# Kernel tuning notes

Measured on AMD Instinct MI355X. Metric: run time of the kernel, lower is better.

## Reference

```python
import jax, jax.numpy as jnp
import numpy as np

EPS = float(np.finfo(np.float32).eps)

# (joint_id, joint_name, parent_name) in the module's fkm_computation_order
ORDER = [
    (1, 'rHip', 'hip'), (2, 'rKnee', 'rHip'), (3, 'rAnkle', 'rKnee'), (4, 'rToe', 'rAnkle'),
    (6, 'lHip', 'hip'), (7, 'lKnee', 'lHip'), (8, 'lAnkle', 'lKnee'), (9, 'lToe', 'lAnkle'),
    (11, 'spine', 'hip'), (12, 'spine1', 'spine'), (13, 'thorax', 'spine1'), (14, 'neck', 'thorax'),
    (15, 'head', 'neck'), (16, 'lShoulderAnchor', 'spine1'), (17, 'lShoulder', 'lShoulderAnchor'),
    (18, 'lElbow', 'lShoulder'), (19, 'lWrist', 'lElbow'), (20, 'lThumb', 'lWrist'),
    (22, 'lWristEnd', 'lWrist'), (24, 'rShoulderAnchor', 'spine1'), (25, 'rShoulder', 'rShoulderAnchor'),
    (26, 'rElbow', 'rShoulder'), (27, 'rWrist', 'rElbow'), (28, 'rThumb', 'rWrist'),
    (30, 'rWristEnd', 'rWrist'),
]


def axis_angle_to_matrix(a):
    """Rodrigues formula, batched. a: [B,3] -> [B,3,3]."""
    theta = jnp.linalg.norm(a, axis=-1, keepdims=True)  # [B,1]
    r = a / (theta + EPS)                               # [B,3]
    r0, r1, r2 = r[:, 0], r[:, 1], r[:, 2]
    z = jnp.zeros_like(r0)
    # skew-symmetric S with S[0,1]=-r2, S[0,2]=r1, S[1,2]=-r0 (as in torch code)
    S = jnp.stack([
        jnp.stack([z, -r2, r1], axis=-1),
        jnp.stack([r2, z, -r0], axis=-1),
        jnp.stack([-r1, r0, z], axis=-1),
    ], axis=-2)  # [B,3,3]
    th = theta[..., None]  # [B,1,1]
    I = jnp.eye(3, dtype=a.dtype)
    return I + jnp.sin(th) * S + (1.0 - jnp.cos(th)) * (S @ S)


def setup_inputs() -> dict:
    key = jax.random.key(0)
    k1, k2 = jax.random.split(key)
    B = 262144
    x = jax.random.normal(k1, (B, 99), dtype=jnp.float32)
    offset = jax.random.normal(k2, (32, 3), dtype=jnp.float32)
    return {"x": x, "offset": offset}


def reference(x, offset):
    # hip root: position from first 3 dims, orientation from dims 3:6
    pos = {"hip": offset[0] + x[:, 0:3]}                # [B,3]
    ang = {"hip": axis_angle_to_matrix(x[:, 3:6])}      # [B,3,3]
    # local rotations for every joint in the chain: dims [3*id+3 : 3*id+6]
    local = {name: axis_angle_to_matrix(x[:, 3 * i + 3: 3 * i + 6]) for i, name, _ in ORDER}
    # sequential forward kinematics down the tree
    for i, cur, par in ORDER:
        # offset[i] @ R_parent  (row-vector times matrix), then translate
        pos[cur] = jnp.einsum('j,bjk->bk', offset[i], ang[par]) + pos[par]
        ang[cur] = local[cur] @ ang[par]
    # positions in the same order as get_joint_positions(): hip then chain order
    return jnp.stack([pos['hip']] + [pos[c] for _, c, _ in ORDER], axis=1)  # [B,26,3]
```

## Files before the change

kernel.cpp:

```cpp
#include <hip/hip_runtime.h>

#define TPB   64
#define RPW   64
#define XDIM  99
#define NJ    26
#define OUTW  78

__device__ __forceinline__ float fast_rcp(float a)  { return __builtin_amdgcn_rcpf(a); }
__device__ __forceinline__ float fast_sqrt(float a) { return __builtin_amdgcn_sqrtf(a); }

__device__ __forceinline__ void rodrigues(float ax, float ay, float az, float* R) {
    const float EPS = 1.1920928955078125e-07f;
    float t = fast_sqrt(ax*ax + ay*ay + az*az);
    float inv = fast_rcp(t + EPS);
    float r0 = ax*inv, r1 = ay*inv, r2 = az*inv;
    float s, c;
    __sincosf(t, &s, &c);
    float omc = 1.0f - c;
    float r00 = r0*r0, r11 = r1*r1, r22 = r2*r2;
    float r01 = r0*r1, r02 = r0*r2, r12 = r1*r2;
    R[0] = 1.0f - omc*(r11 + r22);
    R[1] = -s*r2 + omc*r01;
    R[2] =  s*r1 + omc*r02;
    R[3] =  s*r2 + omc*r01;
    R[4] = 1.0f - omc*(r00 + r22);
    R[5] = -s*r0 + omc*r12;
    R[6] = -s*r1 + omc*r02;
    R[7] =  s*r0 + omc*r12;
    R[8] = 1.0f - omc*(r00 + r11);
}

__global__ __launch_bounds__(TPB, 4) void skel_fk(const float* __restrict__ x,
                                                  const float* __restrict__ off,
                                                  float* __restrict__ out) {
    __shared__ __align__(16) float buf[RPW * XDIM];
    const int l = threadIdx.x;
    const int row0 = blockIdx.x * RPW;
    const float* gsrc = x + (long long)row0 * XDIM;

    #pragma unroll
    for (int j = 0; j < 24; ++j) {
        __builtin_amdgcn_global_load_lds(
            (const __attribute__((address_space(1))) unsigned int*)(gsrc + 256*j + 4*l),
            (__attribute__((address_space(3))) unsigned int*)(buf + 256*j),
            16, 0, 0);
    }
    #pragma unroll
    for (int kk = 0; kk < 3; ++kk) {
        __builtin_amdgcn_global_load_lds(
            (const __attribute__((address_space(1))) unsigned int*)(gsrc + 6144 + 64*kk + l),
            (__attribute__((address_space(3))) unsigned int*)(buf + 6144 + 64*kk),
            4, 0, 0);
    }
    __syncthreads();

    const float* row = &buf[l * XDIM];

    constexpr int OFF_IDX[NJ] = {0,1,2,3,4,6,7,8,9,11,12,13,14,15,16,17,18,19,20,22,24,25,26,27,28,30};
    constexpr int PAR[NJ]     = {-1,0,1,2,3,0,5,6,7,0,9,10,11,12,10,14,15,16,17,17,10,20,21,22,23,23};

    float ang[NJ][9];
    float pp[NJ][3];

    {
        float R[9];
        rodrigues(row[3], row[4], row[5], R);
        #pragma unroll
        for (int q = 0; q < 9; ++q) ang[0][q] = R[q];
        pp[0][0] = off[0] + row[0];
        pp[0][1] = off[1] + row[1];
        pp[0][2] = off[2] + row[2];
    }

    #pragma unroll
    for (int s = 1; s < NJ; ++s) {
        const int i  = OFF_IDX[s];
        const int pa = PAR[s];
        float L[9];
        rodrigues(row[3*i+3], row[3*i+4], row[3*i+5], L);
        const float o0 = off[3*i], o1 = off[3*i+1], o2 = off[3*i+2];
        #pragma unroll
        for (int c = 0; c < 3; ++c)
            pp[s][c] = o0*ang[pa][c] + o1*ang[pa][3+c] + o2*ang[pa][6+c] + pp[pa][c];
        #pragma unroll
        for (int j = 0; j < 3; ++j)
            #pragma unroll
            for (int kk = 0; kk < 3; ++kk)
                ang[s][3*j+kk] = L[3*j+0]*ang[pa][0+kk]
                               + L[3*j+1]*ang[pa][3+kk]
                               + L[3*j+2]*ang[pa][6+kk];
    }
    __syncthreads();

    {
        float2* wr2 = reinterpret_cast<float2*>(buf) + 39 * l;
        #pragma unroll
        for (int j = 0; j < 39; ++j) {
            float2 v;
            v.x = pp[(2*j)   / 3][(2*j)   % 3];
            v.y = pp[(2*j+1) / 3][(2*j+1) % 3];
            wr2[j] = v;
        }
    }
    __syncthreads();

    {
        float4* ob4 = reinterpret_cast<float4*>(out + (long long)row0 * OUTW);
        const float4* b4 = reinterpret_cast<const float4*>(buf);
        #pragma unroll
        for (int j = 0; j < 19; ++j)
            ob4[l + 64*j] = b4[l + 64*j];
        float2* ob2 = reinterpret_cast<float2*>(out + (long long)row0 * OUTW);
        const float2* b2 = reinterpret_cast<const float2*>(buf);
        ob2[2432 + l] = b2[2432 + l];
    }
}

extern "C" void kernel_launch(void* const* d_in, const int* in_sizes, int n_in,
                              void* d_out, int out_size, void* d_ws, size_t ws_size,
                              hipStream_t stream) {
    const float* x   = (const float*)d_in[0];
    const float* off = (const float*)d_in[1];
    float* out = (float*)d_out;
    const int B = in_sizes[0] / XDIM;
    const int grid = B / RPW;
    skel_fk<<<grid, TPB, 0, stream>>>(x, off, out);
}
```

Before: 39.78 us.

## Double-buffer two row slabs per block with manual waitcnt instead of barriers

```diff
diff --git a/kernel.cpp b/kernel.cpp
--- a/kernel.cpp
+++ b/kernel.cpp
@@ -1,10 +1,11 @@
 #include <hip/hip_runtime.h>
 
 #define TPB   64
-#define RPW   64
+#define RPS   64
 #define XDIM  99
 #define NJ    26
 #define OUTW  78
+#define SLABF (RPS * XDIM)
 
 __device__ __forceinline__ float fast_rcp(float a)  { return __builtin_amdgcn_rcpf(a); }
 __device__ __forceinline__ float fast_sqrt(float a) { return __builtin_amdgcn_sqrtf(a); }
@@ -30,35 +31,29 @@
     R[8] = 1.0f - omc*(r00 + r11);
 }
 
-__global__ __launch_bounds__(TPB, 4) void skel_fk(const float* __restrict__ x,
-                                                  const float* __restrict__ off,
-                                                  float* __restrict__ out) {
-    __shared__ __align__(16) float buf[RPW * XDIM];
-    const int l = threadIdx.x;
-    const int row0 = blockIdx.x * RPW;
-    const float* gsrc = x + (long long)row0 * XDIM;
-
+__device__ __forceinline__ void dma_slab(const float* gsrc, float* lbuf, int l) {
     #pragma unroll
     for (int j = 0; j < 24; ++j) {
         __builtin_amdgcn_global_load_lds(
             (const __attribute__((address_space(1))) unsigned int*)(gsrc + 256*j + 4*l),
-            (__attribute__((address_space(3))) unsigned int*)(buf + 256*j),
+            (__attribute__((address_space(3))) unsigned int*)(lbuf + 256*j),
             16, 0, 0);
     }
     #pragma unroll
     for (int kk = 0; kk < 3; ++kk) {
         __builtin_amdgcn_global_load_lds(
             (const __attribute__((address_space(1))) unsigned int*)(gsrc + 6144 + 64*kk + l),
-            (__attribute__((address_space(3))) unsigned int*)(buf + 6144 + 64*kk),
+            (__attribute__((address_space(3))) unsigned int*)(lbuf + 6144 + 64*kk),
             4, 0, 0);
     }
-    __syncthreads();
+}
 
-    const float* row = &buf[l * XDIM];
-
+__device__ __forceinline__ void process_slab(float* slab, float* ob, 
+                                             const float* __restrict__ off, int l) {
     constexpr int OFF_IDX[NJ] = {0,1,2,3,4,6,7,8,9,11,12,13,14,15,16,17,18,19,20,22,24,25,26,27,28,30};
     constexpr int PAR[NJ]     = {-1,0,1,2,3,0,5,6,7,0,9,10,11,12,10,14,15,16,17,17,10,20,21,22,23,23};
 
+    const float* row = &slab[l * XDIM];
     float ang[NJ][9];
     float pp[NJ][3];
 
@@ -71,7 +66,6 @@
         pp[0][1] = off[1] + row[1];
         pp[0][2] = off[2] + row[2];
     }
-
     #pragma unroll
     for (int s = 1; s < NJ; ++s) {
         const int i  = OFF_IDX[s];
@@ -90,10 +84,11 @@
                                + L[3*j+1]*ang[pa][3+kk]
                                + L[3*j+2]*ang[pa][6+kk];
     }
-    __syncthreads();
+
+    asm volatile("" ::: "memory");
 
     {
-        float2* wr2 = reinterpret_cast<float2*>(buf) + 39 * l;
+        float2* wr2 = reinterpret_cast<float2*>(slab) + 39 * l;
         #pragma unroll
         for (int j = 0; j < 39; ++j) {
             float2 v;
@@ -102,18 +97,39 @@
             wr2[j] = v;
         }
     }
-    __syncthreads();
+    asm volatile("s_waitcnt lgkmcnt(0)" ::: "memory");
 
     {
-        float4* ob4 = reinterpret_cast<float4*>(out + (long long)row0 * OUTW);
-        const float4* b4 = reinterpret_cast<const float4*>(buf);
+        float4* ob4 = reinterpret_cast<float4*>(ob);
+        const float4* b4 = reinterpret_cast<const float4*>(slab);
         #pragma unroll
         for (int j = 0; j < 19; ++j)
             ob4[l + 64*j] = b4[l + 64*j];
-        float2* ob2 = reinterpret_cast<float2*>(out + (long long)row0 * OUTW);
-        const float2* b2 = reinterpret_cast<const float2*>(buf);
+        float2* ob2 = reinterpret_cast<float2*>(ob);
+        const float2* b2 = reinterpret_cast<const float2*>(slab);
         ob2[2432 + l] = b2[2432 + l];
     }
+}
+
+__global__ __launch_bounds__(TPB, 4) void skel_fk(const float* __restrict__ x,
+                                                  const float* __restrict__ off,
+                                                  float* __restrict__ out) {
+    __shared__ __align__(16) float buf[2][SLABF];
+    const int l = threadIdx.x;
+    const int row0 = blockIdx.x * (2 * RPS);
+    const float* g0 = x + (long long)row0 * XDIM;
+    const float* g1 = g0 + SLABF;
+    float* o0 = out + (long long)row0 * OUTW;
+    float* o1 = o0 + RPS * OUTW;
+
+    dma_slab(g0, buf[0], l);
+    dma_slab(g1, buf[1], l);
+
+    asm volatile("s_waitcnt vmcnt(27)" ::: "memory");
+    process_slab(buf[0], o0, off, l);
+
+    asm volatile("s_waitcnt vmcnt(12)" ::: "memory");
+    process_slab(buf[1], o1, off, l);
 }
 
 extern "C" void kernel_launch(void* const* d_in, const int* in_sizes, int n_in,
@@ -123,6 +139,6 @@
     const float* off = (const float*)d_in[1];
     float* out = (float*)d_out;
     const int B = in_sizes[0] / XDIM;
-    const int grid = B / RPW;
+    const int grid = B / (2 * RPS);
     skel_fk<<<grid, TPB, 0, stream>>>(x, off, out);
 }
```

After: 47.40 us. +19.1%, slower.

## Halve LDS footprint by staging input columns in two chunks

Applied to the files above, without the earlier changes.

```diff
diff --git a/kernel.cpp b/kernel.cpp
--- a/kernel.cpp
+++ b/kernel.cpp
@@ -1,10 +1,12 @@
 #include <hip/hip_runtime.h>
 
-#define TPB   64
-#define RPW   64
-#define XDIM  99
-#define NJ    26
-#define OUTW  78
+#define TPB  64
+#define RPW  64
+#define XDIM 99
+#define NJ   26
+#define OUTW 78
+#define LSTR 49
+#define CHW  48
 
 __device__ __forceinline__ float fast_rcp(float a)  { return __builtin_amdgcn_rcpf(a); }
 __device__ __forceinline__ float fast_sqrt(float a) { return __builtin_amdgcn_sqrtf(a); }
@@ -33,34 +35,35 @@
 __global__ __launch_bounds__(TPB, 4) void skel_fk(const float* __restrict__ x,
                                                   const float* __restrict__ off,
                                                   float* __restrict__ out) {
-    __shared__ __align__(16) float buf[RPW * XDIM];
+    __shared__ __align__(16) float buf[RPW * LSTR];
     const int l = threadIdx.x;
     const int row0 = blockIdx.x * RPW;
-    const float* gsrc = x + (long long)row0 * XDIM;
+    const float* xb = x + (long long)row0 * XDIM;
 
+    int gb[3], lb[3];
     #pragma unroll
-    for (int j = 0; j < 24; ++j) {
-        __builtin_amdgcn_global_load_lds(
-            (const __attribute__((address_space(1))) unsigned int*)(gsrc + 256*j + 4*l),
-            (__attribute__((address_space(3))) unsigned int*)(buf + 256*j),
-            16, 0, 0);
+    for (int u = 0; u < 3; ++u) {
+        const int m = l + 64 * u;
+        const int r = m / CHW;
+        const int c = m - CHW * r;
+        gb[u] = XDIM * r + c;
+        lb[u] = LSTR * r + c;
     }
-    #pragma unroll
-    for (int kk = 0; kk < 3; ++kk) {
-        __builtin_amdgcn_global_load_lds(
-            (const __attribute__((address_space(1))) unsigned int*)(gsrc + 6144 + 64*kk + l),
-            (__attribute__((address_space(3))) unsigned int*)(buf + 6144 + 64*kk),
-            4, 0, 0);
-    }
-    __syncthreads();
-
-    const float* row = &buf[l * XDIM];
 
     constexpr int OFF_IDX[NJ] = {0,1,2,3,4,6,7,8,9,11,12,13,14,15,16,17,18,19,20,22,24,25,26,27,28,30};
     constexpr int PAR[NJ]     = {-1,0,1,2,3,0,5,6,7,0,9,10,11,12,10,14,15,16,17,17,10,20,21,22,23,23};
 
     float ang[NJ][9];
     float pp[NJ][3];
+
+    const float* row = &buf[l * LSTR];
+
+    #pragma unroll
+    for (int g = 0; g < 16; ++g)
+        #pragma unroll
+        for (int u = 0; u < 3; ++u)
+            buf[196 * g + lb[u]] = xb[396 * g + gb[u]];
+    __syncthreads();
 
     {
         float R[9];
@@ -71,13 +74,13 @@
         pp[0][1] = off[1] + row[1];
         pp[0][2] = off[2] + row[2];
     }
-
     #pragma unroll
-    for (int s = 1; s < NJ; ++s) {
+    for (int s = 1; s <= 12; ++s) {
         const int i  = OFF_IDX[s];
         const int pa = PAR[s];
+        const int col = 3*i + 3;
         float L[9];
-        rodrigues(row[3*i+3], row[3*i+4], row[3*i+5], L);
+        rodrigues(row[col], row[col+1], row[col+2], L);
         const float o0 = off[3*i], o1 = off[3*i+1], o2 = off[3*i+2];
         #pragma unroll
         for (int c = 0; c < 3; ++c)
@@ -92,27 +95,55 @@
     }
     __syncthreads();
 
-    {
-        float2* wr2 = reinterpret_cast<float2*>(buf) + 39 * l;
+    #pragma unroll
+    for (int g = 0; g < 16; ++g)
         #pragma unroll
-        for (int j = 0; j < 39; ++j) {
-            float2 v;
-            v.x = pp[(2*j)   / 3][(2*j)   % 3];
-            v.y = pp[(2*j+1) / 3][(2*j+1) % 3];
-            wr2[j] = v;
-        }
+        for (int u = 0; u < 3; ++u)
+            buf[196 * g + lb[u]] = xb[396 * g + gb[u] + CHW];
+    __syncthreads();
+
+    #pragma unroll
+    for (int s = 13; s < NJ; ++s) {
+        const int i  = OFF_IDX[s];
+        const int pa = PAR[s];
+        const int col = 3*i + 3 - CHW;
+        float L[9];
+        rodrigues(row[col], row[col+1], row[col+2], L);
+        const float o0 = off[3*i], o1 = off[3*i+1], o2 = off[3*i+2];
+        #pragma unroll
+        for (int c = 0; c < 3; ++c)
+            pp[s][c] = o0*ang[pa][c] + o1*ang[pa][3+c] + o2*ang[pa][6+c] + pp[pa][c];
+        #pragma unroll
+        for (int j = 0; j < 3; ++j)
+            #pragma unroll
+            for (int kk = 0; kk < 3; ++kk)
+                ang[s][3*j+kk] = L[3*j+0]*ang[pa][0+kk]
+                               + L[3*j+1]*ang[pa][3+kk]
+                               + L[3*j+2]*ang[pa][6+kk];
     }
     __syncthreads();
 
-    {
-        float4* ob4 = reinterpret_cast<float4*>(out + (long long)row0 * OUTW);
+    float* ob = out + (long long)row0 * OUTW;
+    #pragma unroll
+    for (int g2 = 0; g2 < 2; ++g2) {
+        if (g2) __syncthreads();
+        if ((l >> 5) == g2) {
+            float2* wr2 = reinterpret_cast<float2*>(buf) + 39 * (l & 31);
+            #pragma unroll
+            for (int j = 0; j < 39; ++j) {
+                float2 v;
+                v.x = pp[(2*j)   / 3][(2*j)   % 3];
+                v.y = pp[(2*j+1) / 3][(2*j+1) % 3];
+                wr2[j] = v;
+            }
+        }
+        __syncthreads();
+        float4* ob4 = reinterpret_cast<float4*>(ob + g2 * (32 * OUTW));
         const float4* b4 = reinterpret_cast<const float4*>(buf);
         #pragma unroll
-        for (int j = 0; j < 19; ++j)
+        for (int j = 0; j < 9; ++j)
             ob4[l + 64*j] = b4[l + 64*j];
-        float2* ob2 = reinterpret_cast<float2*>(out + (long long)row0 * OUTW);
-        const float2* b2 = reinterpret_cast<const float2*>(buf);
-        ob2[2432 + l] = b2[2432 + l];
+        if (l < 48) ob4[l + 576] = b4[l + 576];
     }
 }
 
```

Result: slower. 136.5 us (+243.2%).

## Split skeleton FK chains across two wavefronts per row block

Applied to the files above, without the earlier changes.

```diff
diff --git a/kernel.cpp b/kernel.cpp
--- a/kernel.cpp
+++ b/kernel.cpp
@@ -1,10 +1,13 @@
 #include <hip/hip_runtime.h>
 
-#define TPB   64
-#define RPW   64
-#define XDIM  99
-#define NJ    26
-#define OUTW  78
+#define TPB  128
+#define RPW  64
+#define XDIM 99
+#define NJ   26
+#define OUTW 78
+
+constexpr int OFF_IDX[NJ] = {0,1,2,3,4,6,7,8,9,11,12,13,14,15,16,17,18,19,20,22,24,25,26,27,28,30};
+constexpr int PAR[NJ]     = {-1,0,1,2,3,0,5,6,7,0,9,10,11,12,10,14,15,16,17,17,10,20,21,22,23,23};
 
 __device__ __forceinline__ float fast_rcp(float a)  { return __builtin_amdgcn_rcpf(a); }
 __device__ __forceinline__ float fast_sqrt(float a) { return __builtin_amdgcn_sqrtf(a); }
@@ -30,35 +33,63 @@
     R[8] = 1.0f - omc*(r00 + r11);
 }
 
-__global__ __launch_bounds__(TPB, 4) void skel_fk(const float* __restrict__ x,
+#define STEP(s) do {                                                          \
+    const int i_  = OFF_IDX[(s)];                                             \
+    const int pa_ = PAR[(s)];                                                 \
+    float L[9];                                                               \
+    rodrigues(row[3*i_+3], row[3*i_+4], row[3*i_+5], L);                      \
+    const float o0 = off[3*i_], o1 = off[3*i_+1], o2 = off[3*i_+2];           \
+    _Pragma("unroll")                                                         \
+    for (int c = 0; c < 3; ++c)                                               \
+        pp[(s)][c] = o0*ang[pa_][c] + o1*ang[pa_][3+c] + o2*ang[pa_][6+c]     \
+                   + pp[pa_][c];                                              \
+    _Pragma("unroll")                                                         \
+    for (int j = 0; j < 3; ++j)                                               \
+        _Pragma("unroll")                                                     \
+        for (int kk = 0; kk < 3; ++kk)                                        \
+            ang[(s)][3*j+kk] = L[3*j+0]*ang[pa_][0+kk]                        \
+                             + L[3*j+1]*ang[pa_][3+kk]                        \
+                             + L[3*j+2]*ang[pa_][6+kk];                       \
+} while (0)
+
+__global__ __launch_bounds__(TPB, 3) void skel_fk(const float* __restrict__ x,
                                                   const float* __restrict__ off,
                                                   float* __restrict__ out) {
     __shared__ __align__(16) float buf[RPW * XDIM];
-    const int l = threadIdx.x;
+    const int t = threadIdx.x;
+    const int w = t >> 6;
+    const int l = t & 63;
     const int row0 = blockIdx.x * RPW;
     const float* gsrc = x + (long long)row0 * XDIM;
 
-    #pragma unroll
-    for (int j = 0; j < 24; ++j) {
+    if (w == 0) {
+        #pragma unroll
+        for (int j = 0; j < 12; ++j)
+            __builtin_amdgcn_global_load_lds(
+                (const __attribute__((address_space(1))) unsigned int*)(gsrc + 256*j + 4*l),
+                (__attribute__((address_space(3))) unsigned int*)(buf + 256*j),
+                16, 0, 0);
         __builtin_amdgcn_global_load_lds(
-            (const __attribute__((address_space(1))) unsigned int*)(gsrc + 256*j + 4*l),
-            (__attribute__((address_space(3))) unsigned int*)(buf + 256*j),
-            16, 0, 0);
-    }
-    #pragma unroll
-    for (int kk = 0; kk < 3; ++kk) {
-        __builtin_amdgcn_global_load_lds(
-            (const __attribute__((address_space(1))) unsigned int*)(gsrc + 6144 + 64*kk + l),
-            (__attribute__((address_space(3))) unsigned int*)(buf + 6144 + 64*kk),
+            (const __attribute__((address_space(1))) unsigned int*)(gsrc + 6144 + l),
+            (__attribute__((address_space(3))) unsigned int*)(buf + 6144),
             4, 0, 0);
+    } else {
+        #pragma unroll
+        for (int j = 12; j < 24; ++j)
+            __builtin_amdgcn_global_load_lds(
+                (const __attribute__((address_space(1))) unsigned int*)(gsrc + 256*j + 4*l),
+                (__attribute__((address_space(3))) unsigned int*)(buf + 256*j),
+                16, 0, 0);
+        #pragma unroll
+        for (int kk = 1; kk < 3; ++kk)
+            __builtin_amdgcn_global_load_lds(
+                (const __attribute__((address_space(1))) unsigned int*)(gsrc + 6144 + 64*kk + l),
+                (__attribute__((address_space(3))) unsigned int*)(buf + 6144 + 64*kk),
+                4, 0, 0);
     }
     __syncthreads();
 
     const float* row = &buf[l * XDIM];
-
-    constexpr int OFF_IDX[NJ] = {0,1,2,3,4,6,7,8,9,11,12,13,14,15,16,17,18,19,20,22,24,25,26,27,28,30};
-    constexpr int PAR[NJ]     = {-1,0,1,2,3,0,5,6,7,0,9,10,11,12,10,14,15,16,17,17,10,20,21,22,23,23};
-
     float ang[NJ][9];
     float pp[NJ][3];
 
@@ -72,34 +103,38 @@
         pp[0][2] = off[2] + row[2];
     }
 
-    #pragma unroll
-    for (int s = 1; s < NJ; ++s) {
-        const int i  = OFF_IDX[s];
-        const int pa = PAR[s];
-        float L[9];
-        rodrigues(row[3*i+3], row[3*i+4], row[3*i+5], L);
-        const float o0 = off[3*i], o1 = off[3*i+1], o2 = off[3*i+2];
+    if (w == 0) {
         #pragma unroll
-        for (int c = 0; c < 3; ++c)
-            pp[s][c] = o0*ang[pa][c] + o1*ang[pa][3+c] + o2*ang[pa][6+c] + pp[pa][c];
+        for (int s = 1; s <= 13; ++s) STEP(s);
+    } else {
+        STEP(9);
+        STEP(10);
         #pragma unroll
-        for (int j = 0; j < 3; ++j)
-            #pragma unroll
-            for (int kk = 0; kk < 3; ++kk)
-                ang[s][3*j+kk] = L[3*j+0]*ang[pa][0+kk]
-                               + L[3*j+1]*ang[pa][3+kk]
-                               + L[3*j+2]*ang[pa][6+kk];
+        for (int s = 14; s < NJ; ++s) STEP(s);
     }
     __syncthreads();
 
     {
-        float2* wr2 = reinterpret_cast<float2*>(buf) + 39 * l;
-        #pragma unroll
-        for (int j = 0; j < 39; ++j) {
-            float2 v;
-            v.x = pp[(2*j)   / 3][(2*j)   % 3];
-            v.y = pp[(2*j+1) / 3][(2*j+1) % 3];
-            wr2[j] = v;
+        float2* p2 = reinterpret_cast<float2*>(buf);
+        if (w == 0) {
+            float2* wr2 = p2 + 39 * l;
+            #pragma unroll
+            for (int j = 0; j < 21; ++j) {
+                float2 v;
+                v.x = pp[(2*j)   / 3][(2*j)   % 3];
+                v.y = pp[(2*j+1) / 3][(2*j+1) % 3];
+                wr2[j] = v;
+            }
+        } else {
+            float2* wr2 = p2 + 39 * l + 21;
+            #pragma unroll
+            for (int j = 0; j < 18; ++j) {
+                const int f = 42 + 2*j;
+                float2 v;
+                v.x = pp[f / 3][f % 3];
+                v.y = pp[(f+1) / 3][(f+1) % 3];
+                wr2[j] = v;
+            }
         }
     }
     __syncthreads();
@@ -108,11 +143,9 @@
         float4* ob4 = reinterpret_cast<float4*>(out + (long long)row0 * OUTW);
         const float4* b4 = reinterpret_cast<const float4*>(buf);
         #pragma unroll
-        for (int j = 0; j < 19; ++j)
-            ob4[l + 64*j] = b4[l + 64*j];
-        float2* ob2 = reinterpret_cast<float2*>(out + (long long)row0 * OUTW);
-        const float2* b2 = reinterpret_cast<const float2*>(buf);
-        ob2[2432 + l] = b2[2432 + l];
+        for (int j = 0; j < 9; ++j)
+            ob4[t + 128*j] = b4[t + 128*j];
+        if (t < 96) ob4[1152 + t] = b4[1152 + t];
     }
 }
 
```

Result: faster. 37.76 us (-5.1%).
